# Kernel tuning notes

Hardware: AMD Instinct MI355X
Metric: run time of the kernel (lower is better)

Reference implementation:

```python
import jax, jax.numpy as jnp
import numpy as np
from jax import lax

LN_EPS = 1e-6  # flax LayerNorm default


def _layernorm(x, scale, bias):
    mu = jnp.mean(x, axis=-1, keepdims=True)
    var = jnp.mean(jnp.square(x - mu), axis=-1, keepdims=True)
    return (x - mu) * lax.rsqrt(var + LN_EPS) * scale + bias


def _lstm_layer(c0, h0, Wi, Wh, b, x):
    # x: [B, T, F]; carry c/h: [B, H]; gate order i, f, g, o (flax)
    def step(carry, xt):
        c, h = carry
        z = xt @ Wi + h @ Wh + b  # [B, 4H]
        i, f, g, o = jnp.split(z, 4, axis=-1)
        i = jax.nn.sigmoid(i); f = jax.nn.sigmoid(f)
        g = jnp.tanh(g); o = jax.nn.sigmoid(o)
        c = f * c + i * g
        h = o * jnp.tanh(c)
        return (c, h), h
    (cT, hT), hs = lax.scan(step, (c0, h0), jnp.swapaxes(x, 0, 1))
    return cT, hT, jnp.swapaxes(hs, 0, 1)  # hs: [B, T, H]


def setup_inputs() -> dict:
    key = jax.random.key(0)
    ks = jax.random.split(key, 16)
    B, T, F, H, P, A = 64, 128, 512, 1024, 1024, 32
    s = 0.05
    return {
        "x": jax.random.normal(ks[0], (B, T, F), jnp.float32),
        "c0": jnp.zeros((2, B, H), jnp.float32),
        "h0": jnp.zeros((2, B, H), jnp.float32),
        "W_pre": jax.random.normal(ks[1], (F, P), jnp.float32) * s,
        "b_pre": jnp.zeros((P,), jnp.float32),
        "ln_scale": jnp.ones((P,), jnp.float32),
        "ln_bias": jnp.zeros((P,), jnp.float32),
        "Wi0": jax.random.normal(ks[2], (P, 4 * H), jnp.float32) * s,
        "Wh0": jax.random.normal(ks[3], (H, 4 * H), jnp.float32) * s,
        "b0": jnp.zeros((4 * H,), jnp.float32),
        "Wi1": jax.random.normal(ks[4], (H, 4 * H), jnp.float32) * s,
        "Wh1": jax.random.normal(ks[5], (H, 4 * H), jnp.float32) * s,
        "b1": jnp.zeros((4 * H,), jnp.float32),
        "W_post": jax.random.normal(ks[6], (H, P), jnp.float32) * s,
        "b_post": jnp.zeros((P,), jnp.float32),
        "W_out": jax.random.normal(ks[7], (P, A), jnp.float32) * s,
        "b_out": jnp.zeros((A,), jnp.float32),
        "training": False,
    }


def reference(x, c0, h0, W_pre, b_pre, ln_scale, ln_bias,
              Wi0, Wh0, b0, Wi1, Wh1, b1,
              W_post, b_post, W_out, b_out, training):
    # preprocessing: Dense -> LayerNorm -> relu
    h = jax.nn.relu(_layernorm(x @ W_pre + b_pre, ln_scale, ln_bias))
    # two stacked LSTM layers scanned over time
    c1, h1, h = _lstm_layer(c0[0], h0[0], Wi0, Wh0, b0, h)
    c2, h2, h = _lstm_layer(c0[1], h0[1], Wi1, Wh1, b1, h)
    # postprocessing: Dense -> relu (dropout deterministic => identity)
    h = jax.nn.relu(h @ W_post + b_post)
    logits = h @ W_out + b_out  # [B, T, action_dim]
    new_carry = (jnp.stack([c1, c2]), jnp.stack([h1, h2]))
    return new_carry, logits
```

## Files before the change

kernel.cpp:

```cpp
#include <hip/hip_runtime.h>
#include <hip/hip_bf16.h>
#include <math.h>

typedef __attribute__((ext_vector_type(8))) short short8;
typedef __attribute__((ext_vector_type(4))) float f32x4;
typedef __attribute__((ext_vector_type(4))) unsigned u32x4;
typedef unsigned short u16;

__device__ __forceinline__ u16 f2bf(float f) {
    union { float f; unsigned u; } v; v.f = f;
    unsigned r = v.u + 0x7fffu + ((v.u >> 16) & 1u);
    return (u16)(r >> 16);
}
__device__ __forceinline__ float bf2f(u16 b) {
    union { unsigned u; float f; } v; v.u = ((unsigned)b) << 16;
    return v.f;
}
__device__ __forceinline__ float fast_sigmoid(float x) {
    return __builtin_amdgcn_rcpf(1.f + __expf(-x));
}
__device__ __forceinline__ float fast_tanh(float x) {
    return 1.f - 2.f * __builtin_amdgcn_rcpf(1.f + __expf(2.f * x));
}
__device__ __forceinline__ u32x4 ldg16(const void* p) {
    u32x4 r;
    asm volatile("global_load_dwordx4 %0, %1, off"
                 : "=v"(r) : "v"(p) : "memory");
    return r;
}

__device__ __forceinline__ void tr_tile(const float* __restrict__ W,
                                        u16* __restrict__ WT, int K, int N,
                                        int bid, int tid, float (*tile)[33]) {
    int gx = N >> 5;
    int bx = bid % gx, by = bid / gx;
    int n0 = bx * 32, k0 = by * 32;
    int tx = tid & 31, ty = tid >> 5;
    #pragma unroll
    for (int j = 0; j < 32; j += 8)
        tile[ty + j][tx] = W[(size_t)(k0 + ty + j) * N + n0 + tx];
    __syncthreads();
    #pragma unroll
    for (int j = 0; j < 32; j += 8)
        WT[(size_t)(n0 + ty + j) * K + k0 + tx] = f2bf(tile[tx][ty + j]);
}

__global__ __launch_bounds__(256) void k_prep(
    const float* __restrict__ x, u16* __restrict__ Xb,
    const float* __restrict__ h0, u16* __restrict__ hs0, u16* __restrict__ hs1,
    unsigned* __restrict__ ctr,
    const float* __restrict__ Wpre, u16* __restrict__ WTpre,
    const float* __restrict__ Wi0, u16* __restrict__ WTi0,
    const float* __restrict__ Wh0, u16* __restrict__ WTh0,
    const float* __restrict__ Wi1, u16* __restrict__ WTi1,
    const float* __restrict__ Wh1, u16* __restrict__ WTh1,
    const float* __restrict__ Wpost, u16* __restrict__ WTpost,
    const float* __restrict__ Wout, u16* __restrict__ WTout) {
    __shared__ float tile[32][33];
    int bid = blockIdx.x, tid = threadIdx.x;
    if (bid == 0) {
        for (int i = tid; i < 4096; i += 256) ctr[i] = 0u;
        return;
    }
    bid -= 1;
    if (bid < 16384) {
        int i = bid * 256 + tid;
        Xb[i] = f2bf(x[i]);
        return;
    }
    bid -= 16384;
    if (bid < 512) {
        int i = bid * 256 + tid;
        int layer = i >> 16, j = i & 65535;
        int b = j >> 10, jj = j & 1023;
        u16 v = f2bf(h0[(size_t)layer * 65536 + j]);
        u16* dst = layer ? hs1 : hs0;
        dst[(size_t)(jj >> 3) * 512 + b * 8 + (jj & 7)] = v;
        return;
    }
    bid -= 512;
    if (bid < 512)  { tr_tile(Wpre,  WTpre,  512,  1024, bid, tid, tile); return; }
    bid -= 512;
    if (bid < 4096) { tr_tile(Wi0,   WTi0,   1024, 4096, bid, tid, tile); return; }
    bid -= 4096;
    if (bid < 4096) { tr_tile(Wh0,   WTh0,   1024, 4096, bid, tid, tile); return; }
    bid -= 4096;
    if (bid < 4096) { tr_tile(Wi1,   WTi1,   1024, 4096, bid, tid, tile); return; }
    bid -= 4096;
    if (bid < 4096) { tr_tile(Wh1,   WTh1,   1024, 4096, bid, tid, tile); return; }
    bid -= 4096;
    if (bid < 1024) { tr_tile(Wpost, WTpost, 1024, 1024, bid, tid, tile); return; }
    bid -= 1024;
    tr_tile(Wout, WTout, 1024, 32, bid, tid, tile);
}
#define PREP_BLOCKS (1 + 16384 + 512 + 512 + 4 * 4096 + 1024 + 32)

__global__ __launch_bounds__(512) void k_pre(
    const u16* __restrict__ Xb, const u16* __restrict__ WTpre,
    const float* __restrict__ b_pre, const float* __restrict__ ln_s,
    const float* __restrict__ ln_b, u16* __restrict__ preS, int K) {
    __shared__ float zout[16 * 1036];
    __shared__ float lnstat[32];
    const int tid = threadIdx.x;
    const int w = tid >> 6, l = tid & 63, lm = l & 15, lq = l >> 4;
    const int R0 = blockIdx.x * 16;
    const int c0 = w * 128;
    const u16* arow = Xb + (size_t)(R0 + lm) * K + lq * 8;
    const u16* bp = WTpre + (size_t)(c0 + lm) * K + lq * 8;
    f32x4 zv = {0.f, 0.f, 0.f, 0.f};
    f32x4 acc[8] = {zv, zv, zv, zv, zv, zv, zv, zv};
    for (int k0 = 0; k0 < K; k0 += 32) {
        short8 a = *(const short8*)(arow + k0);
        #pragma unroll
        for (int f = 0; f < 8; f++)
            acc[f] = __builtin_amdgcn_mfma_f32_16x16x32_bf16(
                a, *(const short8*)(bp + (size_t)f * 16 * K + k0), acc[f], 0, 0, 0);
    }
    #pragma unroll
    for (int f = 0; f < 8; f++) {
        #pragma unroll
        for (int r = 0; r < 4; r++) {
            int col = c0 + f * 16 + lm;
            zout[(lq * 4 + r) * 1036 + col] = acc[f][r] + b_pre[col];
        }
    }
    __syncthreads();
    {
        int row = tid >> 5, tr = tid & 31;
        float s = 0.f, ss = 0.f;
        #pragma unroll
        for (int j = 0; j < 32; j++) {
            float v = zout[row * 1036 + tr + j * 32];
            s += v; ss += v * v;
        }
        #pragma unroll
        for (int o = 16; o > 0; o >>= 1) {
            s += __shfl_down(s, o, 32);
            ss += __shfl_down(ss, o, 32);
        }
        if (tr == 0) {
            float mu = s * (1.f / 1024.f);
            float var = ss * (1.f / 1024.f) - mu * mu;
            lnstat[row * 2] = mu;
            lnstat[row * 2 + 1] = rsqrtf(var + 1e-6f);
        }
    }
    __syncthreads();
    {
        int row = tid >> 5, tr = tid & 31;
        int R = R0 + row, bb = R >> 7, t = R & 127;
        float mu = lnstat[row * 2], inv = lnstat[row * 2 + 1];
        #pragma unroll
        for (int j = 0; j < 4; j++) {
            int g = tr + j * 32;
            union { u16 h[8]; u32x4 v; } pk;
            #pragma unroll
            for (int e = 0; e < 8; e++) {
                int col = g * 8 + e;
                float v = (zout[row * 1036 + col] - mu) * inv * ln_s[col] + ln_b[col];
                pk.h[e] = f2bf(fmaxf(v, 0.f));
            }
            *(u32x4*)(preS + (size_t)t * 65536 + (size_t)g * 512 + bb * 8) = pk.v;
        }
    }
}

__global__ __launch_bounds__(512) void k_post(
    const u16* __restrict__ Hp, const u16* __restrict__ WTpost,
    const float* __restrict__ b_post, const u16* __restrict__ WTout,
    const float* __restrict__ b_out, float* __restrict__ out, int K) {
    __shared__ u16 pact[16 * 1040];
    const int tid = threadIdx.x;
    const int w = tid >> 6, l = tid & 63, lm = l & 15, lq = l >> 4;
    const int R0 = blockIdx.x * 16;
    const int c0 = w * 128;
    const u16* arow = Hp + (size_t)(R0 + lm) * K + lq * 8;
    const u16* bp = WTpost + (size_t)(c0 + lm) * K + lq * 8;
    f32x4 zv = {0.f, 0.f, 0.f, 0.f};
    f32x4 acc[8] = {zv, zv, zv, zv, zv, zv, zv, zv};
    for (int k0 = 0; k0 < K; k0 += 32) {
        short8 a = *(const short8*)(arow + k0);
        #pragma unroll
        for (int f = 0; f < 8; f++)
            acc[f] = __builtin_amdgcn_mfma_f32_16x16x32_bf16(
                a, *(const short8*)(bp + (size_t)f * 16 * K + k0), acc[f], 0, 0, 0);
    }
    #pragma unroll
    for (int f = 0; f < 8; f++) {
        #pragma unroll
        for (int r = 0; r < 4; r++) {
            int col = c0 + f * 16 + lm;
            float v = acc[f][r] + b_post[col];
            pact[(lq * 4 + r) * 1040 + col] = f2bf(fmaxf(v, 0.f));
        }
    }
    __syncthreads();
    {
        int row = tid >> 5, n = tid & 31;
        const u16* av = pact + row * 1040;
        const u16* wv = WTout + (size_t)n * 1024;
        float s = 0.f;
        for (int k = 0; k < 1024; k += 8) {
            short8 a8 = *(const short8*)(av + k);
            short8 w8 = *(const short8*)(wv + k);
            #pragma unroll
            for (int jj = 0; jj < 8; jj++)
                s += bf2f((u16)a8[jj]) * bf2f((u16)w8[jj]);
        }
        int R = R0 + row, t = R >> 6, bb = R & 63;
        out[262144 + ((size_t)bb * 128 + t) * 32 + n] = s + b_out[n];
    }
}

#define FBLOCKS 256
__global__ __launch_bounds__(512, 1) void k_lstm_fused(
    const u16* __restrict__ WiT0, const u16* __restrict__ WhT0,
    const u16* __restrict__ WiT1, const u16* __restrict__ WhT1,
    const u16* __restrict__ preS, const float* __restrict__ b0v,
    const float* __restrict__ b1v, const float* __restrict__ c0_all,
    u16* __restrict__ hs0, u16* __restrict__ hs1, u16* __restrict__ Hp,
    float* __restrict__ out, unsigned* __restrict__ ctr) {
    const int bk = blockIdx.x;
    const int role = bk >> 7;
    const int bkl = bk & 127;
    const int tid = threadIdx.x;
    const int w = tid >> 6, l = tid & 63, lm = l & 15, lq = l >> 4;
    const int kp = w >> 2, rt = w & 3;

    __shared__ u16 whs[65536];
    __shared__ float zbuf[2 * 64 * 33];
    __shared__ int gflag[2];

    {
        const u16* Wx = role ? WiT1 : WiT0;
        const u16* Wh = role ? WhT1 : WhT0;
        for (int f = tid; f < 8192; f += 512) {
            int flm = f & 15, flq = (f >> 4) & 3;
            int fi = (f >> 6) & 31;
            int rest = f >> 11;
            int fg = rest & 1, fkp = (rest >> 1) & 1;
            int lc = fg * 16 + flm;
            int gcolw = (lc >> 3) * 1024 + bkl * 8 + (lc & 7);
            int k = fi * 32 + flq * 8;
            const u16* src = (fkp == 0 ? Wx : Wh) + (size_t)gcolw * 1024 + k;
            *(short8*)(whs + (size_t)f * 8) = *(const short8*)src;
        }
    }
    if (tid == 0) { gflag[0] = -1; gflag[1] = -1; }
    const int u = tid & 7, b = tid >> 3;
    const int gcol = bkl * 8 + u;
    float c = (c0_all + (size_t)role * 65536)[(size_t)b * 1024 + gcol];
    const float* bv = role ? b1v : b0v;
    float bi0 = bv[gcol], bi1 = bv[1024 + gcol];
    float bi2 = bv[2048 + gcol], bi3 = bv[3072 + gcol];
    u16* hs_my = role ? hs1 : hs0;
    float* c_out = out + (size_t)role * 65536;
    float* h_out = out + 131072 + (size_t)role * 65536;
    const int lanoff = (lq * 16 + lm) * 8;
    __syncthreads();

    for (int t = 0; t < 128; t++) {
        if (role || kp == 1) {
            int need = (role && kp == 0) ? t + 1 : t;
            if (rt == 0) {
                if (need > 0) {
                    int cbase = (role && kp) ? 128 : 0;
                    for (;;) {
                        unsigned a0 = __hip_atomic_load(&ctr[(cbase + l) * 16], __ATOMIC_RELAXED,
                                                        __HIP_MEMORY_SCOPE_AGENT);
                        unsigned a1 = __hip_atomic_load(&ctr[(cbase + 64 + l) * 16], __ATOMIC_RELAXED,
                                                        __HIP_MEMORY_SCOPE_AGENT);
                        if (__all((a0 >= (unsigned)need) && (a1 >= (unsigned)need))) break;
                        __builtin_amdgcn_s_sleep(1);
                    }
                }
                __hip_atomic_store(&gflag[kp], need, __ATOMIC_RELAXED,
                                   __HIP_MEMORY_SCOPE_WORKGROUP);
            } else {
                while (__hip_atomic_load(&gflag[kp], __ATOMIC_RELAXED,
                                         __HIP_MEMORY_SCOPE_WORKGROUP) < need)
                    __builtin_amdgcn_s_sleep(1);
            }
        }

        const u16* abase;
        if (!role) abase = (kp == 0) ? preS + (size_t)t * 65536
                                     : hs0 + (size_t)t * 65536;
        else       abase = (kp == 0) ? hs0 + (size_t)(t + 1) * 65536
                                     : hs1 + (size_t)t * 65536;
        const u16* arow = abase + (size_t)lq * 512 + (rt * 16 + lm) * 8;
        const u16* bw0 = whs + kp * 32768 + lanoff;

        f32x4 zv = {0.f, 0.f, 0.f, 0.f};
        f32x4 ac0[4] = {zv, zv, zv, zv}, ac1[4] = {zv, zv, zv, zv};
        #define STEPF(Ai, i)                                                      \
        {   union { u32x4 q; short8 v; } _a; _a.q = (Ai);                         \
            short8 _b0 = *(const short8*)(bw0 + (i) * 512);                       \
            short8 _b1 = *(const short8*)(bw0 + 16384 + (i) * 512);               \
            ac0[(i) & 3] = __builtin_amdgcn_mfma_f32_16x16x32_bf16(_a.v, _b0, ac0[(i) & 3], 0, 0, 0); \
            ac1[(i) & 3] = __builtin_amdgcn_mfma_f32_16x16x32_bf16(_a.v, _b1, ac1[(i) & 3], 0, 0, 0); }

        u32x4 A0 = ldg16(arow +     0), A1 = ldg16(arow +  2048);
        u32x4 A2 = ldg16(arow +  4096), A3 = ldg16(arow +  6144);
        u32x4 A4 = ldg16(arow +  8192), A5 = ldg16(arow + 10240);
        u32x4 A6 = ldg16(arow + 12288), A7 = ldg16(arow + 14336);
        u32x4 A8 = ldg16(arow + 16384), A9 = ldg16(arow + 18432);
        u32x4 A10 = ldg16(arow + 20480), A11 = ldg16(arow + 22528);
        u32x4 A12 = ldg16(arow + 24576), A13 = ldg16(arow + 26624);
        u32x4 A14 = ldg16(arow + 28672), A15 = ldg16(arow + 30720);
        u32x4 A16 = ldg16(arow + 32768), A17 = ldg16(arow + 34816);
        u32x4 A18 = ldg16(arow + 36864), A19 = ldg16(arow + 38912);
        u32x4 A20 = ldg16(arow + 40960), A21 = ldg16(arow + 43008);
        u32x4 A22 = ldg16(arow + 45056), A23 = ldg16(arow + 47104);
        u32x4 A24 = ldg16(arow + 49152), A25 = ldg16(arow + 51200);
        u32x4 A26 = ldg16(arow + 53248), A27 = ldg16(arow + 55296);
        u32x4 A28 = ldg16(arow + 57344), A29 = ldg16(arow + 59392);
        u32x4 A30 = ldg16(arow + 61440), A31 = ldg16(arow + 63488);
        asm volatile("s_waitcnt vmcnt(24)"
                     : "+v"(A0), "+v"(A1), "+v"(A2), "+v"(A3),
                       "+v"(A4), "+v"(A5), "+v"(A6), "+v"(A7) :: "memory");
        STEPF(A0, 0) STEPF(A1, 1) STEPF(A2, 2) STEPF(A3, 3)
        STEPF(A4, 4) STEPF(A5, 5) STEPF(A6, 6) STEPF(A7, 7)
        asm volatile("s_waitcnt vmcnt(16)"
                     : "+v"(A8), "+v"(A9), "+v"(A10), "+v"(A11),
                       "+v"(A12), "+v"(A13), "+v"(A14), "+v"(A15) :: "memory");
        STEPF(A8, 8) STEPF(A9, 9) STEPF(A10, 10) STEPF(A11, 11)
        STEPF(A12, 12) STEPF(A13, 13) STEPF(A14, 14) STEPF(A15, 15)
        asm volatile("s_waitcnt vmcnt(8)"
                     : "+v"(A16), "+v"(A17), "+v"(A18), "+v"(A19),
                       "+v"(A20), "+v"(A21), "+v"(A22), "+v"(A23) :: "memory");
        STEPF(A16, 16) STEPF(A17, 17) STEPF(A18, 18) STEPF(A19, 19)
        STEPF(A20, 20) STEPF(A21, 21) STEPF(A22, 22) STEPF(A23, 23)
        asm volatile("s_waitcnt vmcnt(0)"
                     : "+v"(A24), "+v"(A25), "+v"(A26), "+v"(A27),
                       "+v"(A28), "+v"(A29), "+v"(A30), "+v"(A31) :: "memory");
        STEPF(A24, 24) STEPF(A25, 25) STEPF(A26, 26) STEPF(A27, 27)
        STEPF(A28, 28) STEPF(A29, 29) STEPF(A30, 30) STEPF(A31, 31)
        #undef STEPF
        f32x4 acc0 = (ac0[0] + ac0[1]) + (ac0[2] + ac0[3]);
        f32x4 acc1 = (ac1[0] + ac1[1]) + (ac1[2] + ac1[3]);

        {
            float* zb = zbuf + (size_t)kp * 2112;
            #pragma unroll
            for (int r = 0; r < 4; r++) {
                int row = rt * 16 + lq * 4 + r;
                zb[row * 33 + lm] = acc0[r];
                zb[row * 33 + 16 + lm] = acc1[r];
            }
        }
        __syncthreads();

        {
            const float* z0 = zbuf + (size_t)b * 33;
            const float* z1 = z0 + 2112;
            float gi = z0[u]      + z1[u]      + bi0;
            float gf = z0[8 + u]  + z1[8 + u]  + bi1;
            float gg = z0[16 + u] + z1[16 + u] + bi2;
            float go = z0[24 + u] + z1[24 + u] + bi3;
            gi = fast_sigmoid(gi);
            gf = fast_sigmoid(gf);
            gg = fast_tanh(gg);
            go = fast_sigmoid(go);
            c = gf * c + gi * gg;
            float h = go * fast_tanh(c);
            unsigned hv = (unsigned)f2bf(h);
            int base = l & 56;
            unsigned p0 = __shfl(hv, base + 0, 64) | (__shfl(hv, base + 1, 64) << 16);
            unsigned p1 = __shfl(hv, base + 2, 64) | (__shfl(hv, base + 3, 64) << 16);
            unsigned p2 = __shfl(hv, base + 4, 64) | (__shfl(hv, base + 5, 64) << 16);
            unsigned p3 = __shfl(hv, base + 6, 64) | (__shfl(hv, base + 7, 64) << 16);
            if (u == 0) {
                u32x4 pv = {p0, p1, p2, p3};
                u16* dst = hs_my + (size_t)(t + 1) * 65536 + (size_t)bkl * 512 + b * 8;
                asm volatile("global_store_dwordx4 %0, %1, off sc0 sc1"
                             :: "v"(dst), "v"(pv) : "memory");
                if (role) {
                    u16* d2 = Hp + (size_t)(t * 64 + b) * 1024 + bkl * 8;
                    *(u32x4*)d2 = pv;
                }
            }
            if (t == 127) {
                c_out[(size_t)b * 1024 + gcol] = c;
                h_out[(size_t)b * 1024 + gcol] = h;
            }
        }
        __syncthreads();

        if (tid == 0)
            __hip_atomic_store(&ctr[bk * 16], (unsigned)(t + 1), __ATOMIC_RELAXED,
                               __HIP_MEMORY_SCOPE_AGENT);
    }
}

extern "C" void kernel_launch(void* const* d_in, const int* in_sizes, int n_in,
                              void* d_out, int out_size, void* d_ws, size_t ws_size,
                              hipStream_t stream) {
    const float* x      = (const float*)d_in[0];
    const float* c0     = (const float*)d_in[1];
    const float* h0     = (const float*)d_in[2];
    const float* W_pre  = (const float*)d_in[3];
    const float* b_pre  = (const float*)d_in[4];
    const float* ln_s   = (const float*)d_in[5];
    const float* ln_b   = (const float*)d_in[6];
    const float* Wi0    = (const float*)d_in[7];
    const float* Wh0    = (const float*)d_in[8];
    const float* b0     = (const float*)d_in[9];
    const float* Wi1    = (const float*)d_in[10];
    const float* Wh1    = (const float*)d_in[11];
    const float* b1     = (const float*)d_in[12];
    const float* W_post = (const float*)d_in[13];
    const float* b_post = (const float*)d_in[14];
    const float* W_out  = (const float*)d_in[15];
    const float* b_out  = (const float*)d_in[16];
    float* out = (float*)d_out;

    char* ws = (char*)d_ws;
    size_t off = 0;
    auto alloc = [&](size_t bytes) {
        void* p = ws + off;
        off += (bytes + 255) & ~(size_t)255;
        return p;
    };
    u16* WTpre  = (u16*)alloc((size_t)1024 * 512 * 2);
    u16* WTi0   = (u16*)alloc((size_t)4096 * 1024 * 2);
    u16* WTh0   = (u16*)alloc((size_t)4096 * 1024 * 2);
    u16* WTi1   = (u16*)alloc((size_t)4096 * 1024 * 2);
    u16* WTh1   = (u16*)alloc((size_t)4096 * 1024 * 2);
    u16* WTpost = (u16*)alloc((size_t)1024 * 1024 * 2);
    u16* WTout  = (u16*)alloc((size_t)32 * 1024 * 2);
    u16* Xb     = (u16*)alloc((size_t)8192 * 512 * 2);
    u16* preS   = (u16*)alloc((size_t)128 * 65536 * 2);
    u16* hs0    = (u16*)alloc((size_t)129 * 65536 * 2);
    u16* hs1    = (u16*)alloc((size_t)129 * 65536 * 2);
    unsigned* ctr = (unsigned*)alloc(32768);
    u16* Hplain = (u16*)alloc((size_t)8192 * 1024 * 2);

    k_prep<<<PREP_BLOCKS, 256, 0, stream>>>(
        x, Xb, h0, hs0, hs1, ctr,
        W_pre, WTpre, Wi0, WTi0, Wh0, WTh0, Wi1, WTi1, Wh1, WTh1,
        W_post, WTpost, W_out, WTout);

    k_pre<<<512, 512, 0, stream>>>(Xb, WTpre, b_pre, ln_s, ln_b, preS, 512);

    {
        const u16* WiT0_ = WTi0; const u16* WhT0_ = WTh0;
        const u16* WiT1_ = WTi1; const u16* WhT1_ = WTh1;
        const u16* preS_ = preS; const float* b0_ = b0; const float* b1_ = b1;
        const float* c0_ = c0; u16* hs0_ = hs0; u16* hs1_ = hs1;
        u16* Hp_ = Hplain; float* out_ = out; unsigned* ctr_ = ctr;
        void* args[] = {&WiT0_, &WhT0_, &WiT1_, &WhT1_, &preS_, &b0_, &b1_,
                        &c0_, &hs0_, &hs1_, &Hp_, &out_, &ctr_};
        hipLaunchCooperativeKernel((void*)k_lstm_fused, dim3(FBLOCKS), dim3(512),
                                   args, 0, stream);
    }

    k_post<<<512, 512, 0, stream>>>(Hplain, WTpost, b_post, WTout, b_out, out, 1024);
}
```

Measured before the change: 1.058 ms.

## Replace block-wide flag wait with per-wave, per-k-chunk readiness polling

Each wave now polls the producer counters itself instead of waiting on a shared-memory flag set by one leader wave. Readiness is tracked per group of 32 producer blocks, which maps to one k-chunk of the activation row. Loads for a chunk start as soon as that chunk's producers are done, so computation can overlap with late producers instead of waiting for all 128. The cost is more global atomic polling traffic from every wave, and finer-grained ordering that depends on relaxed loads.

```diff
diff --git a/kernel.cpp b/kernel.cpp
--- a/kernel.cpp
+++ b/kernel.cpp
@@ -229,7 +229,6 @@
 
     __shared__ u16 whs[65536];
     __shared__ float zbuf[2 * 64 * 33];
-    __shared__ int gflag[2];
 
     {
         const u16* Wx = role ? WiT1 : WiT0;
@@ -246,7 +245,6 @@
             *(short8*)(whs + (size_t)f * 8) = *(const short8*)src;
         }
     }
-    if (tid == 0) { gflag[0] = -1; gflag[1] = -1; }
     const int u = tid & 7, b = tid >> 3;
     const int gcol = bkl * 8 + u;
     float c = (c0_all + (size_t)role * 65536)[(size_t)b * 1024 + gcol];
@@ -260,27 +258,30 @@
     __syncthreads();
 
     for (int t = 0; t < 128; t++) {
-        if (role || kp == 1) {
-            int need = (role && kp == 0) ? t + 1 : t;
-            if (rt == 0) {
-                if (need > 0) {
-                    int cbase = (role && kp) ? 128 : 0;
-                    for (;;) {
-                        unsigned a0 = __hip_atomic_load(&ctr[(cbase + l) * 16], __ATOMIC_RELAXED,
-                                                        __HIP_MEMORY_SCOPE_AGENT);
-                        unsigned a1 = __hip_atomic_load(&ctr[(cbase + 64 + l) * 16], __ATOMIC_RELAXED,
-                                                        __HIP_MEMORY_SCOPE_AGENT);
-                        if (__all((a0 >= (unsigned)need) && (a1 >= (unsigned)need))) break;
-                        __builtin_amdgcn_s_sleep(1);
-                    }
-                }
-                __hip_atomic_store(&gflag[kp], need, __ATOMIC_RELAXED,
-                                   __HIP_MEMORY_SCOPE_WORKGROUP);
-            } else {
-                while (__hip_atomic_load(&gflag[kp], __ATOMIC_RELAXED,
-                                         __HIP_MEMORY_SCOPE_WORKGROUP) < need)
-                    __builtin_amdgcn_s_sleep(1);
-            }
+        unsigned need; int cbase;
+        if (!role) { need = (kp == 1) ? (unsigned)t : 0u; cbase = 0; }
+        else       { need = (kp == 0) ? (unsigned)(t + 1) : (unsigned)t;
+                     cbase = (kp == 0) ? 0 : 128; }
+        unsigned rdy = 0xFu;
+        if (need > 0) {
+            unsigned a0 = __hip_atomic_load(&ctr[(cbase + l) * 16], __ATOMIC_RELAXED,
+                                            __HIP_MEMORY_SCOPE_AGENT);
+            unsigned a1 = __hip_atomic_load(&ctr[(cbase + 64 + l) * 16], __ATOMIC_RELAXED,
+                                            __HIP_MEMORY_SCOPE_AGENT);
+            unsigned long long b0 = __ballot((int)(a0 >= need));
+            unsigned long long b1 = __ballot((int)(a1 >= need));
+            rdy = (((b0 & 0xFFFFFFFFull) == 0xFFFFFFFFull) ? 1u : 0u)
+                | (((b0 >> 32)           == 0xFFFFFFFFull) ? 2u : 0u)
+                | (((b1 & 0xFFFFFFFFull) == 0xFFFFFFFFull) ? 4u : 0u)
+                | (((b1 >> 32)           == 0xFFFFFFFFull) ? 8u : 0u);
+        }
+        #define WAITGRP(g)                                                        \
+        while (!(rdy & (1u << (g)))) {                                            \
+            unsigned e = __hip_atomic_load(                                       \
+                &ctr[(cbase + (g) * 32 + (l & 31)) * 16],                         \
+                __ATOMIC_RELAXED, __HIP_MEMORY_SCOPE_AGENT);                      \
+            if (__all((int)(e >= need))) rdy |= (1u << (g));                      \
+            else __builtin_amdgcn_s_sleep(1);                                     \
         }
 
         const u16* abase;
@@ -300,22 +301,27 @@
             ac0[(i) & 3] = __builtin_amdgcn_mfma_f32_16x16x32_bf16(_a.v, _b0, ac0[(i) & 3], 0, 0, 0); \
             ac1[(i) & 3] = __builtin_amdgcn_mfma_f32_16x16x32_bf16(_a.v, _b1, ac1[(i) & 3], 0, 0, 0); }
 
+        WAITGRP(0)
         u32x4 A0 = ldg16(arow +     0), A1 = ldg16(arow +  2048);
         u32x4 A2 = ldg16(arow +  4096), A3 = ldg16(arow +  6144);
         u32x4 A4 = ldg16(arow +  8192), A5 = ldg16(arow + 10240);
         u32x4 A6 = ldg16(arow + 12288), A7 = ldg16(arow + 14336);
+        WAITGRP(1)
         u32x4 A8 = ldg16(arow + 16384), A9 = ldg16(arow + 18432);
         u32x4 A10 = ldg16(arow + 20480), A11 = ldg16(arow + 22528);
         u32x4 A12 = ldg16(arow + 24576), A13 = ldg16(arow + 26624);
         u32x4 A14 = ldg16(arow + 28672), A15 = ldg16(arow + 30720);
+        WAITGRP(2)
         u32x4 A16 = ldg16(arow + 32768), A17 = ldg16(arow + 34816);
         u32x4 A18 = ldg16(arow + 36864), A19 = ldg16(arow + 38912);
         u32x4 A20 = ldg16(arow + 40960), A21 = ldg16(arow + 43008);
         u32x4 A22 = ldg16(arow + 45056), A23 = ldg16(arow + 47104);
+        WAITGRP(3)
         u32x4 A24 = ldg16(arow + 49152), A25 = ldg16(arow + 51200);
         u32x4 A26 = ldg16(arow + 53248), A27 = ldg16(arow + 55296);
         u32x4 A28 = ldg16(arow + 57344), A29 = ldg16(arow + 59392);
         u32x4 A30 = ldg16(arow + 61440), A31 = ldg16(arow + 63488);
+        #undef WAITGRP
         asm volatile("s_waitcnt vmcnt(24)"
                      : "+v"(A0), "+v"(A1), "+v"(A2), "+v"(A3),
                        "+v"(A4), "+v"(A5), "+v"(A6), "+v"(A7) :: "memory");
```

After: 1.164 ms. 10.1% more time.
